# Kernel tuning notes

Hardware: AMD Instinct MI355X
Metric: run time of the kernel (lower is better)

## Reference

```python
import jax, jax.numpy as jnp
import numpy as np

DIM = 512
HEADS = 8
DIM_HEAD = 64
INNER = HEADS * DIM_HEAD  # 512
B, N = 4, 2048


def setup_inputs() -> dict:
    key = jax.random.key(0)
    k1, k2, k3, k4 = jax.random.split(key, 4)
    x = jax.random.normal(k1, (B, N, DIM), dtype=jnp.float32)
    # nn.Linear(dim, inner*3, bias=False): weight [3*inner, dim]; store transposed [dim, 3*inner]
    w_qkv = jax.random.normal(k2, (DIM, 3 * INNER), dtype=jnp.float32) / np.sqrt(DIM)
    w_out = jax.random.normal(k3, (INNER, DIM), dtype=jnp.float32) / np.sqrt(INNER)
    b_out = jax.random.normal(k4, (DIM,), dtype=jnp.float32) * 0.01
    return {"x": x, "w_qkv": w_qkv, "w_out": w_out, "b_out": b_out}


def reference(x, w_qkv, w_out, b_out):
    b, n, _ = x.shape
    scale = DIM_HEAD ** -0.5
    qkv = x @ w_qkv  # [b, n, 3*inner]
    q, k, v = jnp.split(qkv, 3, axis=-1)
    # [b, n, h, d] -> [b, h, n, d]
    reshape = lambda t: t.reshape(b, n, HEADS, DIM_HEAD).transpose(0, 2, 1, 3)
    q, k, v = reshape(q), reshape(k), reshape(v)
    dots = jnp.einsum('bhid,bhjd->bhij', q, k) * scale  # [b, h, n, n]
    attn = jax.nn.softmax(dots, axis=-1)
    out = jnp.einsum('bhij,bhjd->bhid', attn, v)  # [b, h, n, d]
    out = out.transpose(0, 2, 1, 3).reshape(b, n, INNER)
    return out @ w_out + b_out  # dropout is identity at inference
```

## Files before the change

### kernel.cpp

```cpp
#include <hip/hip_runtime.h>
#include <hip/hip_bf16.h>
#include <cstdint>

#define DEV __device__ __forceinline__

typedef __attribute__((ext_vector_type(8))) __bf16 bf16x8;
typedef __attribute__((ext_vector_type(4))) float floatx4;
typedef __attribute__((ext_vector_type(4))) short shortx4;
typedef __attribute__((ext_vector_type(8))) short shortx8;

constexpr float QSCALE = 0.18033688011112042f;

DEV unsigned short f2b(float f) {
  union { float f; unsigned u; } v; v.f = f;
  return (unsigned short)((v.u + 0x7fffu + ((v.u >> 16) & 1u)) >> 16);
}

#if defined(__has_builtin) && __has_builtin(__builtin_amdgcn_cvt_pk_bf16_f32)
DEV unsigned pk2(float a, float b) {
  typedef __attribute__((ext_vector_type(2))) __bf16 bf2;
  union { bf2 v; unsigned u; } u;
  u.v = __builtin_amdgcn_cvt_pk_bf16_f32(a, b);
  return u.u;
}
#else
DEV unsigned pk2(float a, float b) {
  return (unsigned)f2b(a) | ((unsigned)f2b(b) << 16);
}
#endif

#if defined(__has_builtin) && __has_builtin(__builtin_amdgcn_exp2f)
DEV float fexp2(float x) { return __builtin_amdgcn_exp2f(x); }
#else
DEV float fexp2(float x) { return exp2f(x); }
#endif

DEV floatx4 mfma16(bf16x8 a, bf16x8 b, floatx4 c) {
  return __builtin_amdgcn_mfma_f32_16x16x32_bf16(a, b, c, 0, 0, 0);
}

#define GLD_LDS16(gp, lp)                                                          \
  __builtin_amdgcn_global_load_lds(                                                \
      (const __attribute__((address_space(1))) void*)(gp),                         \
      (__attribute__((address_space(3))) void*)(lp), 16, 0, 0)

__global__ void cvt_f32_bf16(const float* __restrict__ in,
                             unsigned short* __restrict__ out, int n4) {
  int i = blockIdx.x * 256 + threadIdx.x;
  if (i >= n4) return;
  floatx4 f = ((const floatx4*)in)[i];
  shortx4 s;
  s[0] = (short)f2b(f[0]); s[1] = (short)f2b(f[1]);
  s[2] = (short)f2b(f[2]); s[3] = (short)f2b(f[3]);
  ((shortx4*)out)[i] = s;
}

__global__ void tcvt2(const float* __restrict__ w_qkv,
                      const float* __restrict__ w_out,
                      unsigned short* __restrict__ wqkvt,
                      unsigned short* __restrict__ woutt) {
  __shared__ float tile[32][33];
  const float* in; unsigned short* out; int C, bx;
  if (blockIdx.x < 48) { in = w_qkv; out = wqkvt; C = 1536; bx = blockIdx.x; }
  else { in = w_out; out = woutt; C = 512; bx = blockIdx.x - 48; }
  const int R = 512;
  int tx = threadIdx.x & 31, ty = threadIdx.x >> 5;
  int r0 = blockIdx.y * 32, c0 = bx * 32;
#pragma unroll
  for (int i = 0; i < 4; i++) {
    int rr = ty + i * 8;
    tile[rr][tx] = in[(size_t)(r0 + rr) * C + c0 + tx];
  }
  __syncthreads();
#pragma unroll
  for (int i = 0; i < 4; i++) {
    int rr = ty + i * 8;
    out[(size_t)(c0 + rr) * R + r0 + tx] = f2b(tile[tx][rr]);
  }
}

__global__ __launch_bounds__(256, 3) void gemm_qkv(
    const unsigned short* __restrict__ A, const unsigned short* __restrict__ Bt,
    unsigned short* __restrict__ qf, unsigned short* __restrict__ kg,
    unsigned short* __restrict__ vf) {
  __shared__ __align__(16) unsigned short smem[17408];
  const int tid = threadIdx.x;
  const int lane = tid & 63, wid = tid >> 6;
  const int g = lane >> 4, r = lane & 15;
  const int m0 = blockIdx.y * 128, n0 = blockIdx.x * 128;
  const int wm = (wid & 1) * 64, wn = (wid >> 1) * 64;
  const int K = 512;

  floatx4 acc[4][4] = {};

  int rowA[2], kbA[2];
#pragma unroll
  for (int i = 0; i < 2; i++) {
    int c = i * 256 + tid;
    rowA[i] = c >> 2;
    kbA[i] = (c & 3) ^ ((rowA[i] >> 1) & 3);
  }

#define STAGE_G(kt, b)                                                           \
  {                                                                              \
    _Pragma("unroll") for (int i = 0; i < 2; i++) {                              \
      GLD_LDS16(A + (size_t)(m0 + rowA[i]) * K + (kt) + kbA[i] * 8,              \
                (char*)smem + (b)*8192 + i * 4096 + wid * 1024);                 \
      GLD_LDS16(Bt + (size_t)(n0 + rowA[i]) * K + (kt) + kbA[i] * 8,             \
                (char*)smem + 16384 + (b)*8192 + i * 4096 + wid * 1024);         \
    }                                                                            \
  }

  STAGE_G(0, 0)
  for (int it = 0; it < 16; it++) {
    const int buf = it & 1;
    __syncthreads();
    if (it + 1 < 16) STAGE_G((it + 1) * 32, buf ^ 1)
    const unsigned short* Xs = smem + buf * 4096;
    const unsigned short* Ws = smem + 8192 + buf * 4096;
    bf16x8 a[4], b[4];
#pragma unroll
    for (int t = 0; t < 4; t++) {
      int rw = wm + t * 16 + r;
      a[t] = *(const bf16x8*)(Xs + rw * 32 + (g ^ ((rw >> 1) & 3)) * 8);
      int rb = wn + t * 16 + r;
      b[t] = *(const bf16x8*)(Ws + rb * 32 + (g ^ ((rb >> 1) & 3)) * 8);
    }
#pragma unroll
    for (int mt = 0; mt < 4; mt++)
#pragma unroll
      for (int nt = 0; nt < 4; nt++)
        acc[mt][nt] = mfma16(a[mt], b[nt], acc[mt][nt]);
  }
#undef STAGE_G

  const int which = blockIdx.x >> 2;
  if (which == 2) {
    const int tokbase = m0 + wm;
    const int bb = tokbase >> 11, vt = (tokbase & 2047) >> 6;
#pragma unroll
    for (int nt = 0; nt < 4; nt++) {
      int vcol = n0 + wn + nt * 16 + r - 1024;
      int h = vcol >> 6;
      size_t hb = (size_t)(bb * 8 + h) * 131072 + (size_t)vt * 4096 + nt * 1024 +
                  (g * 16 + r) * 8;
#pragma unroll
      for (int kc = 0; kc < 2; kc++) {
        union { unsigned u[4]; shortx8 v; } w;
        w.u[0] = pk2(acc[2 * kc][nt][0], acc[2 * kc][nt][1]);
        w.u[1] = pk2(acc[2 * kc][nt][2], acc[2 * kc][nt][3]);
        w.u[2] = pk2(acc[2 * kc + 1][nt][0], acc[2 * kc + 1][nt][1]);
        w.u[3] = pk2(acc[2 * kc + 1][nt][2], acc[2 * kc + 1][nt][3]);
        *(shortx8*)(vf + hb + kc * 512) = w.v;
      }
    }
  } else {
    const float sc = (which == 0) ? QSCALE : 1.f;
    __syncthreads();
#pragma unroll
    for (int mt = 0; mt < 4; mt++)
#pragma unroll
      for (int nt = 0; nt < 4; nt++) {
        int col = wn + nt * 16 + r;
#pragma unroll
        for (int e = 0; e < 4; e++)
          smem[(wm + mt * 16 + g * 4 + e) * 136 + col] = f2b(acc[mt][nt][e] * sc);
      }
    __syncthreads();
#pragma unroll
    for (int it = 0; it < 8; it++) {
      int c = it * 256 + tid;
      int row = c >> 4, cc = c & 15;
      shortx8 v = *(const shortx8*)(smem + row * 136 + cc * 8);
      int gq = n0 + cc * 8;
      int h = (gq >> 6) & 7, d0 = gq & 63;
      int tok = m0 + row, bb = tok >> 11, n = tok & 2047;
      if (which == 0) {
        int kc = d0 >> 5, gp = (d0 >> 3) & 3;
        *(shortx8*)(qf + (size_t)(bb * 8 + h) * 131072 + (n >> 4) * 1024 +
                    kc * 512 + (gp * 16 + (n & 15)) * 8) = v;
      } else {
        *(shortx8*)(kg + ((size_t)(bb * 8 + h) * 2048 + n) * 64 + d0) = v;
      }
    }
  }
}

__global__ __launch_bounds__(256, 2) void gemm_out(
    const unsigned short* __restrict__ A, const unsigned short* __restrict__ Bt,
    float* __restrict__ outF, const float* __restrict__ bias) {
  __shared__ __align__(16) unsigned short smem[16896];
  const int tid = threadIdx.x;
  const int lane = tid & 63, wid = tid >> 6;
  const int g = lane >> 4, r = lane & 15;
  const int m0 = blockIdx.y * 64, n0 = blockIdx.x * 128;
  const int wn = wid * 32;
  const int K = 512;

  floatx4 acc[4][2] = {};

  const int rA = tid >> 2, kA = (tid & 3) ^ ((rA >> 1) & 3);
  int rB[2], kB[2];
#pragma unroll
  for (int i = 0; i < 2; i++) {
    int c = i * 256 + tid;
    rB[i] = c >> 2;
    kB[i] = (c & 3) ^ ((rB[i] >> 1) & 3);
  }

#define STAGE_O(kt, b)                                                           \
  {                                                                              \
    GLD_LDS16(A + (size_t)(m0 + rA) * K + (kt) + kA * 8,                         \
              (char*)smem + (b)*4096 + wid * 1024);                              \
    _Pragma("unroll") for (int i = 0; i < 2; i++)                                \
        GLD_LDS16(Bt + (size_t)(n0 + rB[i]) * K + (kt) + kB[i] * 8,              \
                  (char*)smem + 8192 + (b)*8192 + i * 4096 + wid * 1024);        \
  }

  STAGE_O(0, 0)
  for (int it = 0; it < 16; it++) {
    const int buf = it & 1;
    __syncthreads();
    if (it + 1 < 16) STAGE_O((it + 1) * 32, buf ^ 1)
    const unsigned short* Xs = smem + buf * 2048;
    const unsigned short* Ws = smem + 4096 + buf * 4096;
    bf16x8 a[4], b[2];
#pragma unroll
    for (int t = 0; t < 4; t++) {
      int rw = t * 16 + r;
      a[t] = *(const bf16x8*)(Xs + rw * 32 + (g ^ ((rw >> 1) & 3)) * 8);
    }
#pragma unroll
    for (int t = 0; t < 2; t++) {
      int rb = wn + t * 16 + r;
      b[t] = *(const bf16x8*)(Ws + rb * 32 + (g ^ ((rb >> 1) & 3)) * 8);
    }
#pragma unroll
    for (int mt = 0; mt < 4; mt++)
#pragma unroll
      for (int bt = 0; bt < 2; bt++)
        acc[mt][bt] = mfma16(a[mt], b[bt], acc[mt][bt]);
  }
#undef STAGE_O

  float* ftile = (float*)smem;
  __syncthreads();
#pragma unroll
  for (int mt = 0; mt < 4; mt++)
#pragma unroll
    for (int bt = 0; bt < 2; bt++)
#pragma unroll
      for (int e = 0; e < 4; e++)
        ftile[(mt * 16 + g * 4 + e) * 132 + wn + bt * 16 + r] = acc[mt][bt][e];
  __syncthreads();
#pragma unroll
  for (int it = 0; it < 8; it++) {
    int c = it * 256 + tid;
    int lr = c >> 5, cc = c & 31;
    floatx4 v = *(const floatx4*)(ftile + lr * 132 + cc * 4);
    int col = n0 + cc * 4;
    v += *(const floatx4*)(bias + col);
    *(floatx4*)(outF + (size_t)(m0 + lr) * 512 + col) = v;
  }
}

__global__ __launch_bounds__(256, 2) void attn(
    const unsigned short* __restrict__ qf, const unsigned short* __restrict__ kg,
    const unsigned short* __restrict__ vf, unsigned short* __restrict__ ao) {
  __shared__ __align__(16) char L[65536];
  unsigned short* Ksm = (unsigned short*)L;
  const int tid = threadIdx.x, lane = tid & 63, wid = tid >> 6;
  const int g = lane >> 4, r = lane & 15, r7 = r & 7;
  const int wq = wid & 1, wk = wid >> 1;
  const int bh = blockIdx.y;
  const size_t kbase = (size_t)bh * (2048 * 64);
  const size_t fbase = (size_t)bh * 131072;
  const unsigned short* vb = vf + fbase;
  const int srow = lane >> 3;
  const int chunk = (lane & 7) ^ (srow & 7);

  const int qt0 = (blockIdx.x * 128 + wq * 64) >> 4;
  bf16x8 bq[4][2];
#pragma unroll
  for (int nt = 0; nt < 4; nt++)
#pragma unroll
    for (int kc = 0; kc < 2; kc++)
      bq[nt][kc] = *(const bf16x8*)(qf + fbase + (size_t)(qt0 + nt) * 1024 +
                                    kc * 512 + lane * 8);

  bf16x8 vones;
#pragma unroll
  for (int i = 0; i < 8; i++) vones[i] = (__bf16)1.0f;

  floatx4 o[4][4] = {};
  floatx4 lacc[4] = {};

#define STAGE_K(rnd, b)                                                          \
  {                                                                              \
    _Pragma("unroll") for (int j = 0; j < 8; j++) {                              \
      int row = (rnd)*256 + wid * 64 + j * 8 + srow;                             \
      GLD_LDS16(kg + kbase + (size_t)row * 64 + chunk * 8,                       \
                (char*)L + (b)*32768 + wid * 8192 + j * 1024);                   \
    }                                                                            \
  }

  STAGE_K(0, 0)
  for (int rnd = 0; rnd < 8; rnd++) {
    const int buf = rnd & 1;
    __syncthreads();
    if (rnd + 1 < 8) STAGE_K(rnd + 1, buf ^ 1)
    const unsigned short* Kt = Ksm + buf * 16384 + (wk * 128) * 64;
#pragma unroll
    for (int sub = 0; sub < 2; sub++) {
      const unsigned short* Ks_ = Kt + sub * 64 * 64;
      const int vt = (rnd * 256 + wk * 128 + sub * 64) >> 6;

      bf16x8 bv[4][2];
#pragma unroll
      for (int b = 0; b < 4; b++)
#pragma unroll
        for (int kc = 0; kc < 2; kc++)
          bv[b][kc] = *(const bf16x8*)(vb + (size_t)vt * 4096 + b * 1024 +
                                       kc * 512 + lane * 8);

      floatx4 st[4][4] = {};
#pragma unroll
      for (int kc = 0; kc < 2; kc++)
#pragma unroll
        for (int mt = 0; mt < 4; mt++) {
          bf16x8 ak = *(const bf16x8*)(Ks_ + (mt * 16 + r) * 64 +
                                       ((kc * 4 + g) ^ r7) * 8);
#pragma unroll
          for (int nt = 0; nt < 4; nt++)
            st[mt][nt] = mfma16(ak, bq[nt][kc], st[mt][nt]);
        }

      bf16x8 ap[4][2];
#pragma unroll
      for (int a = 0; a < 4; a++) {
        float p[4][4];
#pragma unroll
        for (int mt = 0; mt < 4; mt++)
#pragma unroll
          for (int e = 0; e < 4; e++) p[mt][e] = fexp2(st[mt][a][e]);
#pragma unroll
        for (int kc = 0; kc < 2; kc++) {
          union { unsigned u[4]; bf16x8 v; } w;
          w.u[0] = pk2(p[2 * kc][0], p[2 * kc][1]);
          w.u[1] = pk2(p[2 * kc][2], p[2 * kc][3]);
          w.u[2] = pk2(p[2 * kc + 1][0], p[2 * kc + 1][1]);
          w.u[3] = pk2(p[2 * kc + 1][2], p[2 * kc + 1][3]);
          ap[a][kc] = w.v;
        }
      }

#pragma unroll
      for (int kc = 0; kc < 2; kc++)
#pragma unroll
        for (int a = 0; a < 4; a++) {
          lacc[a] = mfma16(ap[a][kc], vones, lacc[a]);
#pragma unroll
          for (int b = 0; b < 4; b++)
            o[a][b] = mfma16(ap[a][kc], bv[b][kc], o[a][b]);
        }
    }
  }
#undef STAGE_K

  float* fP = (float*)L;
  float* fL = (float*)(L + 32768);
  unsigned short* Osm = (unsigned short*)(L + 40960);
  __syncthreads();
  if (wk == 1) {
#pragma unroll
    for (int a = 0; a < 4; a++) {
      *(floatx4*)&fL[wq * 1024 + a * 256 + lane * 4] = lacc[a];
#pragma unroll
      for (int b = 0; b < 4; b++)
        *(floatx4*)&fP[wq * 4096 + (a * 4 + b) * 256 + lane * 4] = o[a][b];
    }
  }
  __syncthreads();
  if (wk == 0) {
#pragma unroll
    for (int a = 0; a < 4; a++) {
      floatx4 lt = lacc[a] + *(floatx4*)&fL[wq * 1024 + a * 256 + lane * 4];
      floatx4 il;
#pragma unroll
      for (int e = 0; e < 4; e++) il[e] = 1.f / lt[e];
#pragma unroll
      for (int b = 0; b < 4; b++) {
        floatx4 oo = o[a][b] +
                     *(floatx4*)&fP[wq * 4096 + (a * 4 + b) * 256 + lane * 4];
#pragma unroll
        for (int e = 0; e < 4; e++)
          Osm[wq * 4608 + (a * 16 + g * 4 + e) * 72 + b * 16 + r] =
              f2b(oo[e] * il[e]);
      }
    }
  }
  __syncthreads();
  const int bb = bh >> 3, h = bh & 7;
#pragma unroll
  for (int it = 0; it < 4; it++) {
    int c = it * 256 + tid;
    int row = c >> 3, cc = c & 7;
    int wqi = row >> 6, r6 = row & 63;
    shortx8 v = *(const shortx8*)(Osm + wqi * 4608 + r6 * 72 + cc * 8);
    int tok = blockIdx.x * 128 + row;
    *(shortx8*)(ao + ((size_t)(bb * 2048 + tok)) * 512 + h * 64 + cc * 8) = v;
  }
}

extern "C" void kernel_launch(void* const* d_in, const int* in_sizes, int n_in,
                              void* d_out, int out_size, void* d_ws, size_t ws_size,
                              hipStream_t stream) {
  const float* x = (const float*)d_in[0];
  const float* w_qkv = (const float*)d_in[1];
  const float* w_out = (const float*)d_in[2];
  const float* b_out = (const float*)d_in[3];
  float* out = (float*)d_out;

  unsigned short* wsp = (unsigned short*)d_ws;
  unsigned short* xb = wsp;
  unsigned short* wqkvt = xb + (size_t)8192 * 512;
  unsigned short* woutt = wqkvt + (size_t)1536 * 512;
  unsigned short* qf = woutt + (size_t)512 * 512;
  unsigned short* kg = qf + (size_t)32 * 2048 * 64;
  unsigned short* vf = kg + (size_t)32 * 2048 * 64;
  unsigned short* ao = vf + (size_t)32 * 2048 * 64;

  cvt_f32_bf16<<<4096, 256, 0, stream>>>(x, xb, 8192 * 512 / 4);
  tcvt2<<<dim3(64, 16), 256, 0, stream>>>(w_qkv, w_out, wqkvt, woutt);
  gemm_qkv<<<dim3(12, 64), 256, 0, stream>>>(xb, wqkvt, qf, kg, vf);
  attn<<<dim3(16, 32), 256, 0, stream>>>(qf, kg, vf, ao);
  gemm_out<<<dim3(4, 128), 256, 0, stream>>>(ao, woutt, out, b_out);
}
```

Measured before the change: 155.1 us.

## Store K in MFMA fragment layout and stream K/V directly from global in attention

```diff
diff --git a/kernel.cpp b/kernel.cpp
--- a/kernel.cpp
+++ b/kernel.cpp
@@ -81,7 +81,7 @@
 
 __global__ __launch_bounds__(256, 3) void gemm_qkv(
     const unsigned short* __restrict__ A, const unsigned short* __restrict__ Bt,
-    unsigned short* __restrict__ qf, unsigned short* __restrict__ kg,
+    unsigned short* __restrict__ qf, unsigned short* __restrict__ kf,
     unsigned short* __restrict__ vf) {
   __shared__ __align__(16) unsigned short smem[17408];
   const int tid = threadIdx.x;
@@ -156,6 +156,7 @@
     }
   } else {
     const float sc = (which == 0) ? QSCALE : 1.f;
+    unsigned short* dst = (which == 0) ? qf : kf;
     __syncthreads();
 #pragma unroll
     for (int mt = 0; mt < 4; mt++)
@@ -174,14 +175,10 @@
       shortx8 v = *(const shortx8*)(smem + row * 136 + cc * 8);
       int gq = n0 + cc * 8;
       int h = (gq >> 6) & 7, d0 = gq & 63;
+      int kc = d0 >> 5, gp = (d0 >> 3) & 3;
       int tok = m0 + row, bb = tok >> 11, n = tok & 2047;
-      if (which == 0) {
-        int kc = d0 >> 5, gp = (d0 >> 3) & 3;
-        *(shortx8*)(qf + (size_t)(bb * 8 + h) * 131072 + (n >> 4) * 1024 +
-                    kc * 512 + (gp * 16 + (n & 15)) * 8) = v;
-      } else {
-        *(shortx8*)(kg + ((size_t)(bb * 8 + h) * 2048 + n) * 64 + d0) = v;
-      }
+      *(shortx8*)(dst + (size_t)(bb * 8 + h) * 131072 + (n >> 4) * 1024 +
+                  kc * 512 + (gp * 16 + (n & 15)) * 8) = v;
     }
   }
 }
@@ -265,139 +262,97 @@
 }
 
 __global__ __launch_bounds__(256, 2) void attn(
-    const unsigned short* __restrict__ qf, const unsigned short* __restrict__ kg,
+    const unsigned short* __restrict__ qf, const unsigned short* __restrict__ kf,
     const unsigned short* __restrict__ vf, unsigned short* __restrict__ ao) {
-  __shared__ __align__(16) char L[65536];
-  unsigned short* Ksm = (unsigned short*)L;
+  __shared__ __align__(16) unsigned short Osm[4][32 * 72];
   const int tid = threadIdx.x, lane = tid & 63, wid = tid >> 6;
-  const int g = lane >> 4, r = lane & 15, r7 = r & 7;
-  const int wq = wid & 1, wk = wid >> 1;
+  const int g = lane >> 4, r = lane & 15;
   const int bh = blockIdx.y;
-  const size_t kbase = (size_t)bh * (2048 * 64);
   const size_t fbase = (size_t)bh * 131072;
+  const unsigned short* kb = kf + fbase;
   const unsigned short* vb = vf + fbase;
-  const int srow = lane >> 3;
-  const int chunk = (lane & 7) ^ (srow & 7);
-
-  const int qt0 = (blockIdx.x * 128 + wq * 64) >> 4;
-  bf16x8 bq[4][2];
-#pragma unroll
-  for (int nt = 0; nt < 4; nt++)
+  const int q0 = blockIdx.x * 128 + wid * 32;
+  const int qt0 = q0 >> 4;
+
+  bf16x8 bq[2][2];
+#pragma unroll
+  for (int nt = 0; nt < 2; nt++)
 #pragma unroll
     for (int kc = 0; kc < 2; kc++)
       bq[nt][kc] = *(const bf16x8*)(qf + fbase + (size_t)(qt0 + nt) * 1024 +
                                     kc * 512 + lane * 8);
 
-  bf16x8 vones;
-#pragma unroll
-  for (int i = 0; i < 8; i++) vones[i] = (__bf16)1.0f;
-
-  floatx4 o[4][4] = {};
-  floatx4 lacc[4] = {};
-
-#define STAGE_K(rnd, b)                                                          \
-  {                                                                              \
-    _Pragma("unroll") for (int j = 0; j < 8; j++) {                              \
-      int row = (rnd)*256 + wid * 64 + j * 8 + srow;                             \
-      GLD_LDS16(kg + kbase + (size_t)row * 64 + chunk * 8,                       \
-                (char*)L + (b)*32768 + wid * 8192 + j * 1024);                   \
-    }                                                                            \
-  }
-
-  STAGE_K(0, 0)
-  for (int rnd = 0; rnd < 8; rnd++) {
-    const int buf = rnd & 1;
-    __syncthreads();
-    if (rnd + 1 < 8) STAGE_K(rnd + 1, buf ^ 1)
-    const unsigned short* Kt = Ksm + buf * 16384 + (wk * 128) * 64;
-#pragma unroll
-    for (int sub = 0; sub < 2; sub++) {
-      const unsigned short* Ks_ = Kt + sub * 64 * 64;
-      const int vt = (rnd * 256 + wk * 128 + sub * 64) >> 6;
-
-      bf16x8 bv[4][2];
-#pragma unroll
-      for (int b = 0; b < 4; b++)
-#pragma unroll
-        for (int kc = 0; kc < 2; kc++)
-          bv[b][kc] = *(const bf16x8*)(vb + (size_t)vt * 4096 + b * 1024 +
-                                       kc * 512 + lane * 8);
-
-      floatx4 st[4][4] = {};
+  floatx4 o[2][4] = {};
+  float lsum[2] = {0.f, 0.f};
+
+  for (int s = 0; s < 32; s++) {
+    const size_t kt = (size_t)s * 4096;
+    bf16x8 ak[4][2], bv[4][2];
+#pragma unroll
+    for (int mt = 0; mt < 4; mt++)
 #pragma unroll
       for (int kc = 0; kc < 2; kc++)
-#pragma unroll
-        for (int mt = 0; mt < 4; mt++) {
-          bf16x8 ak = *(const bf16x8*)(Ks_ + (mt * 16 + r) * 64 +
-                                       ((kc * 4 + g) ^ r7) * 8);
-#pragma unroll
-          for (int nt = 0; nt < 4; nt++)
-            st[mt][nt] = mfma16(ak, bq[nt][kc], st[mt][nt]);
-        }
-
-      bf16x8 ap[4][2];
-#pragma unroll
-      for (int a = 0; a < 4; a++) {
-        float p[4][4];
+        ak[mt][kc] = *(const bf16x8*)(kb + kt + mt * 1024 + kc * 512 + lane * 8);
+#pragma unroll
+    for (int b = 0; b < 4; b++)
+#pragma unroll
+      for (int kc = 0; kc < 2; kc++)
+        bv[b][kc] = *(const bf16x8*)(vb + kt + b * 1024 + kc * 512 + lane * 8);
+
+#pragma unroll
+    for (int nt = 0; nt < 2; nt++) {
+      floatx4 st[4] = {};
+#pragma unroll
+      for (int kc = 0; kc < 2; kc++)
 #pragma unroll
         for (int mt = 0; mt < 4; mt++)
-#pragma unroll
-          for (int e = 0; e < 4; e++) p[mt][e] = fexp2(st[mt][a][e]);
-#pragma unroll
-        for (int kc = 0; kc < 2; kc++) {
-          union { unsigned u[4]; bf16x8 v; } w;
-          w.u[0] = pk2(p[2 * kc][0], p[2 * kc][1]);
-          w.u[1] = pk2(p[2 * kc][2], p[2 * kc][3]);
-          w.u[2] = pk2(p[2 * kc + 1][0], p[2 * kc + 1][1]);
-          w.u[3] = pk2(p[2 * kc + 1][2], p[2 * kc + 1][3]);
-          ap[a][kc] = w.v;
-        }
+          st[mt] = mfma16(ak[mt][kc], bq[nt][kc], st[mt]);
+
+      float p[4][4];
+#pragma unroll
+      for (int mt = 0; mt < 4; mt++)
+#pragma unroll
+        for (int e = 0; e < 4; e++) p[mt][e] = fexp2(st[mt][e]);
+      lsum[nt] += ((p[0][0] + p[0][1]) + (p[0][2] + p[0][3])) +
+                  ((p[1][0] + p[1][1]) + (p[1][2] + p[1][3])) +
+                  ((p[2][0] + p[2][1]) + (p[2][2] + p[2][3])) +
+                  ((p[3][0] + p[3][1]) + (p[3][2] + p[3][3]));
+      bf16x8 ap[2];
+#pragma unroll
+      for (int kc = 0; kc < 2; kc++) {
+        union { unsigned u[4]; bf16x8 v; } w;
+        w.u[0] = pk2(p[2 * kc][0], p[2 * kc][1]);
+        w.u[1] = pk2(p[2 * kc][2], p[2 * kc][3]);
+        w.u[2] = pk2(p[2 * kc + 1][0], p[2 * kc + 1][1]);
+        w.u[3] = pk2(p[2 * kc + 1][2], p[2 * kc + 1][3]);
+        ap[kc] = w.v;
       }
 
 #pragma unroll
       for (int kc = 0; kc < 2; kc++)
 #pragma unroll
-        for (int a = 0; a < 4; a++) {
-          lacc[a] = mfma16(ap[a][kc], vones, lacc[a]);
-#pragma unroll
-          for (int b = 0; b < 4; b++)
-            o[a][b] = mfma16(ap[a][kc], bv[b][kc], o[a][b]);
-        }
-    }
-  }
-#undef STAGE_K
-
-  float* fP = (float*)L;
-  float* fL = (float*)(L + 32768);
-  unsigned short* Osm = (unsigned short*)(L + 40960);
-  __syncthreads();
-  if (wk == 1) {
-#pragma unroll
-    for (int a = 0; a < 4; a++) {
-      *(floatx4*)&fL[wq * 1024 + a * 256 + lane * 4] = lacc[a];
-#pragma unroll
-      for (int b = 0; b < 4; b++)
-        *(floatx4*)&fP[wq * 4096 + (a * 4 + b) * 256 + lane * 4] = o[a][b];
-    }
-  }
-  __syncthreads();
-  if (wk == 0) {
-#pragma unroll
-    for (int a = 0; a < 4; a++) {
-      floatx4 lt = lacc[a] + *(floatx4*)&fL[wq * 1024 + a * 256 + lane * 4];
-      floatx4 il;
-#pragma unroll
-      for (int e = 0; e < 4; e++) il[e] = 1.f / lt[e];
-#pragma unroll
-      for (int b = 0; b < 4; b++) {
-        floatx4 oo = o[a][b] +
-                     *(floatx4*)&fP[wq * 4096 + (a * 4 + b) * 256 + lane * 4];
-#pragma unroll
-        for (int e = 0; e < 4; e++)
-          Osm[wq * 4608 + (a * 16 + g * 4 + e) * 72 + b * 16 + r] =
-              f2b(oo[e] * il[e]);
-      }
-    }
+        for (int b = 0; b < 4; b++)
+          o[nt][b] = mfma16(ap[kc], bv[b][kc], o[nt][b]);
+    }
+  }
+
+#pragma unroll
+  for (int nt = 0; nt < 2; nt++) {
+    lsum[nt] += __shfl_xor(lsum[nt], 16);
+    lsum[nt] += __shfl_xor(lsum[nt], 32);
+  }
+
+#pragma unroll
+  for (int nt = 0; nt < 2; nt++) {
+    float il[4];
+#pragma unroll
+    for (int e = 0; e < 4; e++) il[e] = 1.f / __shfl(lsum[nt], g * 4 + e);
+#pragma unroll
+    for (int b = 0; b < 4; b++)
+#pragma unroll
+      for (int e = 0; e < 4; e++)
+        Osm[wid][(nt * 16 + g * 4 + e) * 72 + b * 16 + r] =
+            f2b(o[nt][b][e] * il[e]);
   }
   __syncthreads();
   const int bb = bh >> 3, h = bh & 7;
@@ -405,8 +360,8 @@
   for (int it = 0; it < 4; it++) {
     int c = it * 256 + tid;
     int row = c >> 3, cc = c & 7;
-    int wqi = row >> 6, r6 = row & 63;
-    shortx8 v = *(const shortx8*)(Osm + wqi * 4608 + r6 * 72 + cc * 8);
+    int w = row >> 5, r5 = row & 31;
+    shortx8 v = *(const shortx8*)(&Osm[w][r5 * 72 + cc * 8]);
     int tok = blockIdx.x * 128 + row;
     *(shortx8*)(ao + ((size_t)(bb * 2048 + tok)) * 512 + h * 64 + cc * 8) = v;
   }
@@ -426,13 +381,13 @@
   unsigned short* wqkvt = xb + (size_t)8192 * 512;
   unsigned short* woutt = wqkvt + (size_t)1536 * 512;
   unsigned short* qf = woutt + (size_t)512 * 512;
-  unsigned short* kg = qf + (size_t)32 * 2048 * 64;
-  unsigned short* vf = kg + (size_t)32 * 2048 * 64;
+  unsigned short* kf = qf + (size_t)32 * 2048 * 64;
+  unsigned short* vf = kf + (size_t)32 * 2048 * 64;
   unsigned short* ao = vf + (size_t)32 * 2048 * 64;
 
   cvt_f32_bf16<<<4096, 256, 0, stream>>>(x, xb, 8192 * 512 / 4);
   tcvt2<<<dim3(64, 16), 256, 0, stream>>>(w_qkv, w_out, wqkvt, woutt);
-  gemm_qkv<<<dim3(12, 64), 256, 0, stream>>>(xb, wqkvt, qf, kg, vf);
-  attn<<<dim3(16, 32), 256, 0, stream>>>(qf, kg, vf, ao);
+  gemm_qkv<<<dim3(12, 64), 256, 0, stream>>>(xb, wqkvt, qf, kf, vf);
+  attn<<<dim3(16, 32), 256, 0, stream>>>(qf, kf, vf, ao);
   gemm_out<<<dim3(4, 128), 256, 0, stream>>>(ao, woutt, out, b_out);
 }
```

Result: slower. 188.5 us (+21.5%).
